# Kernel optimization log

Measured on AMD Instinct MI355X. Metric: run time of the kernel, lower is better.

Reference implementation:

```python
import jax, jax.numpy as jnp
import numpy as np

UNITS = 1024
LEVELS = 16
CHUNK = UNITS // LEVELS  # 64


def cumsoftmax(x, mode):
    # softmax then cumsum along last axis; 'r2l' reverses before/after
    if mode == 'l2r':
        return jnp.cumsum(jax.nn.softmax(x, axis=-1), axis=-1)
    else:  # 'r2l'
        xr = x[..., ::-1]
        return jnp.cumsum(jax.nn.softmax(xr, axis=-1), axis=-1)[..., ::-1]


def setup_inputs() -> dict:
    key = jax.random.key(0)
    k1, k2, k3 = jax.random.split(key, 3)
    B, T, D = 32, 512, 1024
    G = UNITS * 4 + LEVELS * 2  # 4128
    x = jax.random.normal(k1, (B, T, D), dtype=jnp.float32)
    kernel = jax.random.normal(k2, (D, G), dtype=jnp.float32) * (1.0 / np.sqrt(D))
    recurrent_kernel = jax.random.normal(k3, (UNITS, G), dtype=jnp.float32) * (1.0 / np.sqrt(UNITS))
    bias = jnp.zeros((G,), dtype=jnp.float32)
    return {"x": x, "kernel": kernel, "recurrent_kernel": recurrent_kernel, "bias": bias}


def reference(x, kernel, recurrent_kernel, bias):
    B, T, D = x.shape
    L, U, C = LEVELS, UNITS, CHUNK

    def one_step(carry, x_t):
        c_last, h_last = carry  # [B, U] each
        z = x_t @ kernel + h_last @ recurrent_kernel + bias  # [B, 4U+2L]
        f_master = cumsoftmax(z[:, :L], 'l2r')[:, :, None]       # [B, L, 1]
        i_master = cumsoftmax(z[:, L:2 * L], 'r2l')[:, :, None]  # [B, L, 1]
        g = z[:, 2 * L:].reshape(B, 4 * L, C)
        f_gate = jax.nn.sigmoid(g[:, :L])
        i_gate = jax.nn.sigmoid(g[:, L:2 * L])
        o_gate = jax.nn.sigmoid(g[:, 2 * L:3 * L])
        c_in = jnp.tanh(g[:, 3 * L:])
        c_prev = c_last.reshape(B, L, C)
        overlap = f_master * i_master
        c_out = (overlap * (f_gate * c_prev + i_gate * c_in)
                 + (f_master - overlap) * c_prev
                 + (i_master - overlap) * c_in)
        h_out = (o_gate * jnp.tanh(c_out)).reshape(B, U)
        c_out = c_out.reshape(B, U)
        return (c_out, h_out), h_out

    init = (jnp.zeros((B, U), x.dtype), jnp.zeros((B, U), x.dtype))
    _, h_seq = jax.lax.scan(one_step, init, jnp.swapaxes(x, 0, 1))  # [T, B, U]
    return jnp.swapaxes(h_seq, 0, 1)  # [B, T, U] (return_sequences=True)
```

## Files before the change

kernel.cpp:

```cpp
#include <hip/hip_runtime.h>

#define TT 512
#define GG 4128
#define GPAD 4224
#define NBLK2 64
#define NTHR2 512

typedef _Float16 f16;
typedef _Float16 half8 __attribute__((ext_vector_type(8)));
typedef _Float16 half4 __attribute__((ext_vector_type(4)));
typedef float f32x4 __attribute__((ext_vector_type(4)));
typedef unsigned long long ull;

__device__ __forceinline__ half8 h8(uint4 v) {
  union { uint4 u; half8 h; } c; c.u = v; return c.h;
}

__global__ void k_transpose_cvt(const float* __restrict__ in, f16* __restrict__ out,
                                int R, int C) {
  __shared__ float tile[32][33];
  int bx = blockIdx.x * 32, by = blockIdx.y * 32;
  int tx = threadIdx.x & 31, ty = threadIdx.x >> 5;
#pragma unroll
  for (int j = 0; j < 4; ++j) {
    int r = by + ty + j * 8;
    tile[ty + j * 8][tx] = in[(long)r * C + bx + tx];
  }
  __syncthreads();
#pragma unroll
  for (int j = 0; j < 4; ++j) {
    int c = bx + ty + j * 8;
    out[(long)c * R + by + tx] = (f16)tile[tx][ty + j * 8];
  }
}

__global__ __launch_bounds__(256) void k_gemm_xw(
    const float* __restrict__ X,
    const f16* __restrict__ Bt,
    const float* __restrict__ bias,
    f16* __restrict__ Zm,
    f16* __restrict__ Zg) {
  __shared__ f16 As[128 * 32];
  __shared__ f16 Bs[128 * 32];
  const int m0 = blockIdx.x * 128;
  const int n0 = blockIdx.y * 128;
  const int tid = threadIdx.x;
  const int wave = tid >> 6, lane = tid & 63;
  const int mrow = (wave & 1) * 64, ncol = (wave >> 1) * 64;
  f32x4 acc[4][4];
#pragma unroll
  for (int i = 0; i < 4; ++i)
#pragma unroll
    for (int j = 0; j < 4; ++j)
      acc[i][j] = (f32x4){0.f, 0.f, 0.f, 0.f};

  float4 ra[4];
  uint4 rb[2];
  auto load_tiles = [&](int k0) {
#pragma unroll
    for (int q = 0; q < 4; ++q) {
      int flat = q * 256 + tid;
      int r = flat >> 3, s = flat & 7;
      ra[q] = *(const float4*)(X + (long)(m0 + r) * 1024 + k0 + s * 4);
    }
#pragma unroll
    for (int q = 0; q < 2; ++q) {
      int flat = q * 256 + tid;
      int r = flat >> 2, s = flat & 3;
      rb[q] = *(const uint4*)(Bt + (long)(n0 + r) * 1024 + k0 + s * 8);
    }
  };
  load_tiles(0);
  for (int kt = 0; kt < 32; ++kt) {
    __syncthreads();
#pragma unroll
    for (int q = 0; q < 4; ++q) {
      int flat = q * 256 + tid;
      half4 h;
      h[0] = (f16)ra[q].x; h[1] = (f16)ra[q].y;
      h[2] = (f16)ra[q].z; h[3] = (f16)ra[q].w;
      *(half4*)((char*)As + flat * 8) = h;
    }
#pragma unroll
    for (int q = 0; q < 2; ++q) {
      int flat = q * 256 + tid;
      *(uint4*)((char*)Bs + flat * 16) = rb[q];
    }
    __syncthreads();
    if (kt + 1 < 32) load_tiles((kt + 1) * 32);
    const int kseg2 = ((lane >> 4) * 8) * 2;
    half8 af[4], bf[4];
#pragma unroll
    for (int i = 0; i < 4; ++i) {
      int r = mrow + i * 16 + (lane & 15);
      af[i] = *(const half8*)((const char*)As + r * 64 + kseg2);
      int c = ncol + i * 16 + (lane & 15);
      bf[i] = *(const half8*)((const char*)Bs + c * 64 + kseg2);
    }
#pragma unroll
    for (int i = 0; i < 4; ++i)
#pragma unroll
      for (int j = 0; j < 4; ++j)
        acc[i][j] = __builtin_amdgcn_mfma_f32_16x16x32_f16(af[i], bf[j], acc[i][j], 0, 0, 0);
  }
#pragma unroll
  for (int j = 0; j < 4; ++j) {
    int n = n0 + ncol + j * 16 + (lane & 15);
    if (n < GG) {
      float bv = bias[n];
      const int isM = (n < 32);
      int q = 0, u4 = 0, g2 = 0;
      if (!isM) {
        int k = n - 32;
        q = k >> 10;
        int u = k & 1023;
        g2 = u >> 4;
        u4 = u & 15;
      }
#pragma unroll
      for (int i = 0; i < 4; ++i) {
#pragma unroll
        for (int r = 0; r < 4; ++r) {
          int m = m0 + mrow + i * 16 + (lane >> 4) * 4 + r;
          int b = m >> 9, tt2 = m & 511;
          f16 v = (f16)(acc[i][j][r] + bv);
          if (isM)
            Zm[((long)(tt2 * 32 + b)) * 32 + n] = v;
          else
            Zg[((((long)tt2 * 64 + g2) * 32 + b) * 16 + u4) * 4 + q] = v;
        }
      }
    }
  }
}

__device__ __forceinline__ float sigm(float x) { return 1.f / (1.f + __expf(-x)); }
__device__ __forceinline__ float tanh_(float x) {
  float ax = fabsf(x);
  float e = __expf(-2.f * ax);
  float t = (1.f - e) / (1.f + e);
  return copysignf(t, x);
}
#define AG_LD(p) __hip_atomic_load((p), __ATOMIC_RELAXED, __HIP_MEMORY_SCOPE_AGENT)
#define AG_ST(p, v) __hip_atomic_store((p), (v), __ATOMIC_RELAXED, __HIP_MEMORY_SCOPE_AGENT)

__device__ __forceinline__ void bar_lds() {
  asm volatile("s_waitcnt lgkmcnt(0)" ::: "memory");
  __builtin_amdgcn_sched_barrier(0);
  __builtin_amdgcn_s_barrier();
  __builtin_amdgcn_sched_barrier(0);
}

__global__ __launch_bounds__(NTHR2, 2) void k_onlstm(
    const f16* __restrict__ Zm, const f16* __restrict__ Zg,
    const f16* __restrict__ Rt, unsigned* __restrict__ hbuf,
    unsigned* __restrict__ flags, float* __restrict__ Y) {
  extern __shared__ char lds[];
  float* cumlds = (float*)(lds + 32768);
  const int g = blockIdx.x, tid = threadIdx.x;
  const int wave = tid >> 6, lane = tid & 63;
  const int lr = lane & 15, lq = lane >> 4;
  const int kq = wave;
  const int b = tid >> 4;
  const int u = tid & 15;
  const int L0 = g >> 2;
  const int side = tid >> 5, mb = tid & 31;

  uint4 bq[16], bm[8];
  {
    const f16* base = Rt + (long)kq * 128 + lq * 8;
#pragma unroll
    for (int q = 0; q < 4; ++q)
#pragma unroll
      for (int ks = 0; ks < 4; ++ks)
        bq[q * 4 + ks] = *(const uint4*)(base + (long)(32 + q * 1024 + g * 16 + lr) * 1024 + ks * 32);
#pragma unroll
    for (int ct = 0; ct < 2; ++ct)
#pragma unroll
      for (int ks = 0; ks < 4; ++ks)
        bm[ct * 4 + ks] = *(const uint4*)(base + (long)(ct * 16 + lr) * 1024 + ks * 32);
#pragma unroll
    for (int i = 0; i < 16; ++i)
      asm volatile("" : "+v"(bq[i].x), "+v"(bq[i].y), "+v"(bq[i].z), "+v"(bq[i].w));
#pragma unroll
    for (int i = 0; i < 8; ++i)
      asm volatile("" : "+v"(bm[i].x), "+v"(bm[i].y), "+v"(bm[i].z), "+v"(bm[i].w));
  }
  float creg = 0.f;

  for (int t = 0; t < TT; ++t) {
    half4 zxh = *(const half4*)(Zg + ((((long)t * 64 + g) * 32 + b) * 16 + u) * 4);
    half8 zmr0, zmr1;
    if (wave == 0) {
      const half8* zmp = (const half8*)(Zm + ((long)t * 32 + mb) * 32 + side * 16);
      zmr0 = zmp[0];
      zmr1 = zmp[1];
    }
    if (t > 0) {
      for (;;) {
        unsigned v = AG_LD(flags + lane * 16);
        if (__all((int)(v >= (unsigned)t))) break;
      }
    }
    const ull* hrd = (const ull*)hbuf + (t & 1) * 8192;
    ull hv[16];
#pragma unroll
    for (int it = 0; it < 16; ++it)
      hv[it] = AG_LD(hrd + it * 512 + tid);
    __builtin_amdgcn_sched_barrier(0);
#pragma unroll
    for (int it = 0; it < 16; ++it) {
      int idx = it * 512 + tid;
      int bb = idx >> 8, j8 = idx & 255;
      *(ull*)(lds + ((bb * 128 + ((j8 >> 1) ^ (bb & 7))) << 4) + (j8 & 1) * 8) = hv[it];
    }
    bar_lds();
    f32x4 acc[4][2], accm[2][2];
#pragma unroll
    for (int q = 0; q < 4; ++q) {
      acc[q][0] = (f32x4){0.f, 0.f, 0.f, 0.f};
      acc[q][1] = (f32x4){0.f, 0.f, 0.f, 0.f};
    }
#pragma unroll
    for (int ct = 0; ct < 2; ++ct) {
      accm[ct][0] = (f32x4){0.f, 0.f, 0.f, 0.f};
      accm[ct][1] = (f32x4){0.f, 0.f, 0.f, 0.f};
    }
#pragma unroll
    for (int ks = 0; ks < 4; ++ks) {
      int ch = kq * 16 + ks * 4 + lq;
      half8 a0 = *(const half8*)(lds + ((lr * 128 + (ch ^ (lr & 7))) << 4));
      half8 a1 = *(const half8*)(lds + (((16 + lr) * 128 + (ch ^ ((16 + lr) & 7))) << 4));
#pragma unroll
      for (int q = 0; q < 4; ++q) {
        acc[q][0] = __builtin_amdgcn_mfma_f32_16x16x32_f16(a0, h8(bq[q * 4 + ks]), acc[q][0], 0, 0, 0);
        acc[q][1] = __builtin_amdgcn_mfma_f32_16x16x32_f16(a1, h8(bq[q * 4 + ks]), acc[q][1], 0, 0, 0);
      }
#pragma unroll
      for (int ct = 0; ct < 2; ++ct) {
        accm[ct][0] = __builtin_amdgcn_mfma_f32_16x16x32_f16(a0, h8(bm[ct * 4 + ks]), accm[ct][0], 0, 0, 0);
        accm[ct][1] = __builtin_amdgcn_mfma_f32_16x16x32_f16(a1, h8(bm[ct * 4 + ks]), accm[ct][1], 0, 0, 0);
      }
    }
#pragma unroll
    for (int q = 0; q < 4; ++q)
#pragma unroll
      for (int bt = 0; bt < 2; ++bt) {
        int bsw = (bt * 16 + lq * 4) ^ ((lr & 7) << 2);
        *(f32x4*)(lds + 65536 + (((kq * 64 + q * 16 + lr) * 32 + bsw) << 2)) = acc[q][bt];
      }
    bar_lds();
#pragma unroll
    for (int ct = 0; ct < 2; ++ct)
#pragma unroll
      for (int bt = 0; bt < 2; ++bt) {
        int col = ct * 16 + lr;
        int bsw = (bt * 16 + lq * 4) ^ ((col & 7) << 2);
        *(f32x4*)(lds + (((kq * 32 + col) * 32 + bsw) << 2)) = accm[ct][bt];
      }
    float z[4];
#pragma unroll
    for (int q = 0; q < 4; ++q) {
      float s = 0.f;
      int bsw = b ^ ((u & 7) << 2);
#pragma unroll
      for (int k8 = 0; k8 < 8; ++k8)
        s += *(const float*)(lds + 65536 + (((k8 * 64 + q * 16 + u) * 32 + bsw) << 2));
      z[q] = s + (float)zxh[q];
    }
    float f = sigm(z[0]), i_ = sigm(z[1]), o = sigm(z[2]);
    float ci = tanh_(z[3]);
    bar_lds();
    if (wave == 0) {
      float v[16];
#pragma unroll
      for (int j = 0; j < 16; ++j) {
        int col = side * 16 + j;
        int bsw = mb ^ ((col & 7) << 2);
        float s = 0.f;
#pragma unroll
        for (int k8 = 0; k8 < 8; ++k8)
          s += *(const float*)(lds + (((k8 * 32 + col) * 32 + bsw) << 2));
        v[j] = s + (float)((j < 8) ? zmr0[j] : zmr1[j - 8]);
      }
      float mx = v[0];
#pragma unroll
      for (int j = 1; j < 16; ++j) mx = fmaxf(mx, v[j]);
      float ssum = 0.f, p = 0.f;
#pragma unroll
      for (int j = 0; j < 16; ++j) {
        float e = __expf(v[j] - mx);
        ssum += e;
        bool take = side ? (j >= L0) : (j <= L0);
        if (take) p += e;
      }
      cumlds[side * 32 + mb] = p / ssum;
    }
    bar_lds();
    float fm = cumlds[b], im = cumlds[32 + b];
    float ov = fm * im;
    float cn = ov * (f * creg + i_ * ci) + (fm - ov) * creg + (im - ov) * ci;
    creg = cn;
    float hval = o * tanh_(cn);
    float hp = __shfl_xor(hval, 1);
    if (!(u & 1)) {
      union { f16 h[2]; unsigned w; } pk;
      pk.h[0] = (f16)hval;
      pk.h[1] = (f16)hp;
      AG_ST(hbuf + ((t + 1) & 1) * 16384 + b * 512 + g * 8 + (u >> 1), pk.w);
    }
    asm volatile("s_waitcnt vmcnt(0)" ::: "memory");
    __builtin_amdgcn_s_barrier();
    if (tid == 0) AG_ST(flags + g * 16, (unsigned)(t + 1));
    Y[((long)b * TT + t) * 1024 + g * 16 + u] = hval;
  }
}

extern "C" void kernel_launch(void* const* d_in, const int* in_sizes, int n_in,
                              void* d_out, int out_size, void* d_ws, size_t ws_size,
                              hipStream_t stream) {
  const float* X = (const float*)d_in[0];
  const float* W = (const float*)d_in[1];
  const float* Rm = (const float*)d_in[2];
  const float* bias = (const float*)d_in[3];
  float* Y = (float*)d_out;
  char* ws = (char*)d_ws;

  const size_t off_flags = 0;
  const size_t off_h = 4096;
  const size_t off_Zm = 135168;
  const size_t off_Wt = 1183744;
  const size_t off_Rt = 9834496;
  const size_t off_Zg = 18288640;
  const size_t need = off_Zg + (size_t)TT * 64 * 32 * 16 * 4 * 2;
  if (ws_size < need) return;

  unsigned* flags = (unsigned*)(ws + off_flags);
  unsigned* hbuf = (unsigned*)(ws + off_h);
  f16* Zm = (f16*)(ws + off_Zm);
  f16* Wt = (f16*)(ws + off_Wt);
  f16* Rt = (f16*)(ws + off_Rt);
  f16* Zg = (f16*)(ws + off_Zg);

  hipMemsetAsync(ws, 0, 135168, stream);
  hipMemsetAsync(ws + off_Wt + (size_t)GG * 1024 * 2, 0, (size_t)(GPAD - GG) * 1024 * 2, stream);

  k_transpose_cvt<<<dim3(129, 32), 256, 0, stream>>>(W, Wt, 1024, GG);
  k_transpose_cvt<<<dim3(129, 32), 256, 0, stream>>>(Rm, Rt, 1024, GG);
  k_gemm_xw<<<dim3(128, 33), 256, 0, stream>>>(X, Wt, bias, Zm, Zg);

  hipFuncSetAttribute((const void*)k_onlstm, hipFuncAttributeMaxDynamicSharedMemorySize, 131072);
  k_onlstm<<<NBLK2, NTHR2, 131072, stream>>>(Zm, Zg, Rt, hbuf, flags, Y);
}
```

Before: 4.204 ms.

## Embed step tags in hidden-state words to replace flag-based grid sync

Drops the per-block flag array and the barrier-then-flag publish. Each thread now writes its hidden value as an fp32 word whose low 8 mantissa bits carry the step tag. Readers spin on coherent dwordx4 loads of the whole hidden buffer until every tag matches. This removes a full block barrier, a store drain and a separate flag round trip from each recurrent step. In exchange it doubles the hidden-state traffic (fp32 instead of fp16), re-reads the whole buffer on every spin, and slightly truncates precision.

```diff
diff --git a/kernel.cpp b/kernel.cpp
--- a/kernel.cpp
+++ b/kernel.cpp
@@ -10,10 +10,18 @@
 typedef _Float16 half8 __attribute__((ext_vector_type(8)));
 typedef _Float16 half4 __attribute__((ext_vector_type(4)));
 typedef float f32x4 __attribute__((ext_vector_type(4)));
+typedef unsigned u32x4 __attribute__((ext_vector_type(4)));
 typedef unsigned long long ull;
 
 __device__ __forceinline__ half8 h8(uint4 v) {
   union { uint4 u; half8 h; } c; c.u = v; return c.h;
+}
+
+__device__ __forceinline__ u32x4 ld_cohx4(const unsigned* p) {
+  u32x4 r;
+  asm volatile("global_load_dwordx4 %0, %1, off sc0 sc1"
+               : "=v"(r) : "v"(p) : "memory");
+  return r;
 }
 
 __global__ void k_transpose_cvt(const float* __restrict__ in, f16* __restrict__ out,
@@ -141,7 +149,6 @@
   float t = (1.f - e) / (1.f + e);
   return copysignf(t, x);
 }
-#define AG_LD(p) __hip_atomic_load((p), __ATOMIC_RELAXED, __HIP_MEMORY_SCOPE_AGENT)
 #define AG_ST(p, v) __hip_atomic_store((p), (v), __ATOMIC_RELAXED, __HIP_MEMORY_SCOPE_AGENT)
 
 __device__ __forceinline__ void bar_lds() {
@@ -153,8 +160,8 @@
 
 __global__ __launch_bounds__(NTHR2, 2) void k_onlstm(
     const f16* __restrict__ Zm, const f16* __restrict__ Zg,
-    const f16* __restrict__ Rt, unsigned* __restrict__ hbuf,
-    unsigned* __restrict__ flags, float* __restrict__ Y) {
+    const f16* __restrict__ Rt, unsigned* __restrict__ hbuf32,
+    float* __restrict__ Y) {
   extern __shared__ char lds[];
   float* cumlds = (float*)(lds + 32768);
   const int g = blockIdx.x, tid = threadIdx.x;
@@ -196,23 +203,31 @@
       zmr0 = zmp[0];
       zmr1 = zmp[1];
     }
-    if (t > 0) {
-      for (;;) {
-        unsigned v = AG_LD(flags + lane * 16);
-        if (__all((int)(v >= (unsigned)t))) break;
-      }
-    }
-    const ull* hrd = (const ull*)hbuf + (t & 1) * 8192;
-    ull hv[16];
-#pragma unroll
-    for (int it = 0; it < 16; ++it)
-      hv[it] = AG_LD(hrd + it * 512 + tid);
-    __builtin_amdgcn_sched_barrier(0);
+    const unsigned* hb = hbuf32 + (t & 1) * 32768;
+    const unsigned tg = (unsigned)(t & 0xFF);
+    u32x4 hw[16];
+    for (;;) {
+#pragma unroll
+      for (int it = 0; it < 16; ++it)
+        hw[it] = ld_cohx4(hb + (it * 512 + tid) * 4);
+      asm volatile("s_waitcnt vmcnt(0)" ::: "memory");
+      __builtin_amdgcn_sched_barrier(0);
+      unsigned bad = 0;
+#pragma unroll
+      for (int it = 0; it < 16; ++it)
+        bad |= (hw[it].x ^ tg) | (hw[it].y ^ tg) | (hw[it].z ^ tg) | (hw[it].w ^ tg);
+      if (__all((int)((bad & 0xFFu) == 0u))) break;
+    }
 #pragma unroll
     for (int it = 0; it < 16; ++it) {
       int idx = it * 512 + tid;
       int bb = idx >> 8, j8 = idx & 255;
-      *(ull*)(lds + ((bb * 128 + ((j8 >> 1) ^ (bb & 7))) << 4) + (j8 & 1) * 8) = hv[it];
+      half4 hh;
+      hh[0] = (f16)__uint_as_float(hw[it].x);
+      hh[1] = (f16)__uint_as_float(hw[it].y);
+      hh[2] = (f16)__uint_as_float(hw[it].z);
+      hh[3] = (f16)__uint_as_float(hw[it].w);
+      *(half4*)(lds + ((bb * 128 + ((j8 >> 1) ^ (bb & 7))) << 4) + (j8 & 1) * 8) = hh;
     }
     bar_lds();
     f32x4 acc[4][2], accm[2][2];
@@ -302,16 +317,8 @@
     float cn = ov * (f * creg + i_ * ci) + (fm - ov) * creg + (im - ov) * ci;
     creg = cn;
     float hval = o * tanh_(cn);
-    float hp = __shfl_xor(hval, 1);
-    if (!(u & 1)) {
-      union { f16 h[2]; unsigned w; } pk;
-      pk.h[0] = (f16)hval;
-      pk.h[1] = (f16)hp;
-      AG_ST(hbuf + ((t + 1) & 1) * 16384 + b * 512 + g * 8 + (u >> 1), pk.w);
-    }
-    asm volatile("s_waitcnt vmcnt(0)" ::: "memory");
-    __builtin_amdgcn_s_barrier();
-    if (tid == 0) AG_ST(flags + g * 16, (unsigned)(t + 1));
+    unsigned hword = (__float_as_uint(hval) & 0xFFFFFF00u) | ((unsigned)(t + 1) & 0xFFu);
+    AG_ST(hbuf32 + ((t + 1) & 1) * 32768 + b * 1024 + g * 16 + u, hword);
     Y[((long)b * TT + t) * 1024 + g * 16 + u] = hval;
   }
 }
@@ -326,23 +333,21 @@
   float* Y = (float*)d_out;
   char* ws = (char*)d_ws;
 
-  const size_t off_flags = 0;
-  const size_t off_h = 4096;
-  const size_t off_Zm = 135168;
-  const size_t off_Wt = 1183744;
-  const size_t off_Rt = 9834496;
-  const size_t off_Zg = 18288640;
+  const size_t off_h = 0;
+  const size_t off_Zm = 262144;
+  const size_t off_Wt = 1310720;
+  const size_t off_Rt = 9961472;
+  const size_t off_Zg = 18415616;
   const size_t need = off_Zg + (size_t)TT * 64 * 32 * 16 * 4 * 2;
   if (ws_size < need) return;
 
-  unsigned* flags = (unsigned*)(ws + off_flags);
-  unsigned* hbuf = (unsigned*)(ws + off_h);
+  unsigned* hbuf32 = (unsigned*)(ws + off_h);
   f16* Zm = (f16*)(ws + off_Zm);
   f16* Wt = (f16*)(ws + off_Wt);
   f16* Rt = (f16*)(ws + off_Rt);
   f16* Zg = (f16*)(ws + off_Zg);
 
-  hipMemsetAsync(ws, 0, 135168, stream);
+  hipMemsetAsync(ws + off_h, 0, 262144, stream);
   hipMemsetAsync(ws + off_Wt + (size_t)GG * 1024 * 2, 0, (size_t)(GPAD - GG) * 1024 * 2, stream);
 
   k_transpose_cvt<<<dim3(129, 32), 256, 0, stream>>>(W, Wt, 1024, GG);
@@ -350,5 +355,5 @@
   k_gemm_xw<<<dim3(128, 33), 256, 0, stream>>>(X, Wt, bias, Zm, Zg);
 
   hipFuncSetAttribute((const void*)k_onlstm, hipFuncAttributeMaxDynamicSharedMemorySize, 131072);
-  k_onlstm<<<NBLK2, NTHR2, 131072, stream>>>(Zm, Zg, Rt, hbuf, flags, Y);
-}
+  k_onlstm<<<NBLK2, NTHR2, 131072, stream>>>(Zm, Zg, Rt, hbuf32, Y);
+}
```

After: 3.833 ms. 1.1x faster.

## Load recurrent h straight into MFMA registers and compute master gates in every thread

Applied to the files above, without the earlier changes.

Each wave now reads its MFMA A-operand fragments of h directly from global memory using coherent dwordx4 loads, so the LDS staging of h and its barrier are gone. The master-gate reductions are now spread across all threads and written to LDS. Every thread then recomputes the two 16-wide cumsoftmax values for its batch row instead of having wave 0 compute them and broadcast them. This removes one block barrier per timestep and the serial wave-0 softmax section on the recurrent critical path, at the cost of redundant exp work and more global load traffic per wave.

```diff
diff --git a/kernel.cpp b/kernel.cpp
--- a/kernel.cpp
+++ b/kernel.cpp
@@ -10,10 +10,21 @@
 typedef _Float16 half8 __attribute__((ext_vector_type(8)));
 typedef _Float16 half4 __attribute__((ext_vector_type(4)));
 typedef float f32x4 __attribute__((ext_vector_type(4)));
+typedef unsigned u32x4 __attribute__((ext_vector_type(4)));
 typedef unsigned long long ull;
 
 __device__ __forceinline__ half8 h8(uint4 v) {
   union { uint4 u; half8 h; } c; c.u = v; return c.h;
+}
+__device__ __forceinline__ half8 h8v(u32x4 v) {
+  union { u32x4 u; half8 h; } c; c.u = v; return c.h;
+}
+
+__device__ __forceinline__ u32x4 ld_cohx4(const unsigned* p) {
+  u32x4 r;
+  asm volatile("global_load_dwordx4 %0, %1, off sc0 sc1"
+               : "=v"(r) : "v"(p) : "memory");
+  return r;
 }
 
 __global__ void k_transpose_cvt(const float* __restrict__ in, f16* __restrict__ out,
@@ -154,9 +165,8 @@
 __global__ __launch_bounds__(NTHR2, 2) void k_onlstm(
     const f16* __restrict__ Zm, const f16* __restrict__ Zg,
     const f16* __restrict__ Rt, unsigned* __restrict__ hbuf,
-    unsigned* __restrict__ flags, float* __restrict__ Y) {
+    unsigned* __restrict__ flagbuf, float* __restrict__ Y) {
   extern __shared__ char lds[];
-  float* cumlds = (float*)(lds + 32768);
   const int g = blockIdx.x, tid = threadIdx.x;
   const int wave = tid >> 6, lane = tid & 63;
   const int lr = lane & 15, lq = lane >> 4;
@@ -164,21 +174,21 @@
   const int b = tid >> 4;
   const int u = tid & 15;
   const int L0 = g >> 2;
-  const int side = tid >> 5, mb = tid & 31;
+  const int rb_ = tid & 31, rc = tid >> 5;
 
   uint4 bq[16], bm[8];
   {
-    const f16* base = Rt + (long)kq * 128 + lq * 8;
+    const f16* baseg = Rt + (long)kq * 128 + lq * 8;
 #pragma unroll
     for (int q = 0; q < 4; ++q)
 #pragma unroll
       for (int ks = 0; ks < 4; ++ks)
-        bq[q * 4 + ks] = *(const uint4*)(base + (long)(32 + q * 1024 + g * 16 + lr) * 1024 + ks * 32);
+        bq[q * 4 + ks] = *(const uint4*)(baseg + (long)(32 + q * 1024 + g * 16 + lr) * 1024 + ks * 32);
 #pragma unroll
     for (int ct = 0; ct < 2; ++ct)
 #pragma unroll
       for (int ks = 0; ks < 4; ++ks)
-        bm[ct * 4 + ks] = *(const uint4*)(base + (long)(ct * 16 + lr) * 1024 + ks * 32);
+        bm[ct * 4 + ks] = *(const uint4*)(baseg + (long)(ct * 16 + lr) * 1024 + ks * 32);
 #pragma unroll
     for (int i = 0; i < 16; ++i)
       asm volatile("" : "+v"(bq[i].x), "+v"(bq[i].y), "+v"(bq[i].z), "+v"(bq[i].w));
@@ -187,34 +197,29 @@
       asm volatile("" : "+v"(bm[i].x), "+v"(bm[i].y), "+v"(bm[i].z), "+v"(bm[i].w));
   }
   float creg = 0.f;
+  const int wb0 = lr * 512 + kq * 64 + lq * 4;
+  const int wb1 = (lr + 16) * 512 + kq * 64 + lq * 4;
 
   for (int t = 0; t < TT; ++t) {
     half4 zxh = *(const half4*)(Zg + ((((long)t * 64 + g) * 32 + b) * 16 + u) * 4);
-    half8 zmr0, zmr1;
-    if (wave == 0) {
-      const half8* zmp = (const half8*)(Zm + ((long)t * 32 + mb) * 32 + side * 16);
-      zmr0 = zmp[0];
-      zmr1 = zmp[1];
-    }
+    f16 zm0 = Zm[((long)t * 32 + rb_) * 32 + rc];
+    f16 zm1 = Zm[((long)t * 32 + rb_) * 32 + rc + 16];
     if (t > 0) {
+      const unsigned tg = (unsigned)t;
       for (;;) {
-        unsigned v = AG_LD(flags + lane * 16);
-        if (__all((int)(v >= (unsigned)t))) break;
-      }
-    }
-    const ull* hrd = (const ull*)hbuf + (t & 1) * 8192;
-    ull hv[16];
-#pragma unroll
-    for (int it = 0; it < 16; ++it)
-      hv[it] = AG_LD(hrd + it * 512 + tid);
+        unsigned v = AG_LD(flagbuf + lane * 16);
+        if (__all((int)(v >= tg))) break;
+      }
+    }
+    const unsigned* hb = hbuf + (t & 1) * 16384;
+    u32x4 ha[8];
+#pragma unroll
+    for (int ks = 0; ks < 4; ++ks) {
+      ha[ks] = ld_cohx4(hb + wb0 + ks * 16);
+      ha[4 + ks] = ld_cohx4(hb + wb1 + ks * 16);
+    }
+    asm volatile("s_waitcnt vmcnt(0)" ::: "memory");
     __builtin_amdgcn_sched_barrier(0);
-#pragma unroll
-    for (int it = 0; it < 16; ++it) {
-      int idx = it * 512 + tid;
-      int bb = idx >> 8, j8 = idx & 255;
-      *(ull*)(lds + ((bb * 128 + ((j8 >> 1) ^ (bb & 7))) << 4) + (j8 & 1) * 8) = hv[it];
-    }
-    bar_lds();
     f32x4 acc[4][2], accm[2][2];
 #pragma unroll
     for (int q = 0; q < 4; ++q) {
@@ -228,9 +233,8 @@
     }
 #pragma unroll
     for (int ks = 0; ks < 4; ++ks) {
-      int ch = kq * 16 + ks * 4 + lq;
-      half8 a0 = *(const half8*)(lds + ((lr * 128 + (ch ^ (lr & 7))) << 4));
-      half8 a1 = *(const half8*)(lds + (((16 + lr) * 128 + (ch ^ ((16 + lr) & 7))) << 4));
+      half8 a0 = h8v(ha[ks]);
+      half8 a1 = h8v(ha[4 + ks]);
 #pragma unroll
       for (int q = 0; q < 4; ++q) {
         acc[q][0] = __builtin_amdgcn_mfma_f32_16x16x32_f16(a0, h8(bq[q * 4 + ks]), acc[q][0], 0, 0, 0);
@@ -247,57 +251,64 @@
 #pragma unroll
       for (int bt = 0; bt < 2; ++bt) {
         int bsw = (bt * 16 + lq * 4) ^ ((lr & 7) << 2);
-        *(f32x4*)(lds + 65536 + (((kq * 64 + q * 16 + lr) * 32 + bsw) << 2)) = acc[q][bt];
+        *(f32x4*)(lds + (((kq * 64 + q * 16 + lr) * 32 + bsw) << 2)) = acc[q][bt];
+      }
+#pragma unroll
+    for (int ct = 0; ct < 2; ++ct)
+#pragma unroll
+      for (int bt = 0; bt < 2; ++bt) {
+        int colm = ct * 16 + lr;
+        int bsw = (bt * 16 + lq * 4) ^ ((colm & 7) << 2);
+        *(f32x4*)(lds + 65536 + (((kq * 32 + colm) * 32 + bsw) << 2)) = accm[ct][bt];
       }
     bar_lds();
-#pragma unroll
-    for (int ct = 0; ct < 2; ++ct)
-#pragma unroll
-      for (int bt = 0; bt < 2; ++bt) {
-        int col = ct * 16 + lr;
-        int bsw = (bt * 16 + lq * 4) ^ ((col & 7) << 2);
-        *(f32x4*)(lds + (((kq * 32 + col) * 32 + bsw) << 2)) = accm[ct][bt];
-      }
     float z[4];
-#pragma unroll
-    for (int q = 0; q < 4; ++q) {
+    {
+      int bswg = b ^ ((u & 7) << 2);
+#pragma unroll
+      for (int q = 0; q < 4; ++q) {
+        float s = 0.f;
+#pragma unroll
+        for (int k8 = 0; k8 < 8; ++k8)
+          s += *(const float*)(lds + (((k8 * 64 + q * 16 + u) * 32 + bswg) << 2));
+        z[q] = s + (float)zxh[q];
+      }
+    }
+#pragma unroll
+    for (int rep = 0; rep < 2; ++rep) {
+      int c = rc + rep * 16;
+      int bswm = rb_ ^ ((c & 7) << 2);
       float s = 0.f;
-      int bsw = b ^ ((u & 7) << 2);
 #pragma unroll
       for (int k8 = 0; k8 < 8; ++k8)
-        s += *(const float*)(lds + 65536 + (((k8 * 64 + q * 16 + u) * 32 + bsw) << 2));
-      z[q] = s + (float)zxh[q];
-    }
+        s += *(const float*)(lds + 65536 + (((k8 * 32 + c) * 32 + bswm) << 2));
+      s += (float)(rep ? zm1 : zm0);
+      *(float*)(lds + 98304 + ((c * 32 + bswm) << 2)) = s;
+    }
+    bar_lds();
+    float vf[16], vi[16];
+#pragma unroll
+    for (int j = 0; j < 16; ++j) {
+      int bsw = b ^ ((j & 7) << 2);
+      vf[j] = *(const float*)(lds + 98304 + (((j * 32) + bsw) << 2));
+      vi[j] = *(const float*)(lds + 98304 + ((((16 + j) * 32) + bsw) << 2));
+    }
+    float mf = vf[0], mi = vi[0];
+#pragma unroll
+    for (int j = 1; j < 16; ++j) { mf = fmaxf(mf, vf[j]); mi = fmaxf(mi, vi[j]); }
+    float sf = 0.f, pf = 0.f, si = 0.f, pi = 0.f;
+#pragma unroll
+    for (int j = 0; j < 16; ++j) {
+      float ef = __expf(vf[j] - mf);
+      sf += ef;
+      if (j <= L0) pf += ef;
+      float ei = __expf(vi[j] - mi);
+      si += ei;
+      if (j >= L0) pi += ei;
+    }
+    float fm = pf / sf, im = pi / si;
     float f = sigm(z[0]), i_ = sigm(z[1]), o = sigm(z[2]);
     float ci = tanh_(z[3]);
-    bar_lds();
-    if (wave == 0) {
-      float v[16];
-#pragma unroll
-      for (int j = 0; j < 16; ++j) {
-        int col = side * 16 + j;
-        int bsw = mb ^ ((col & 7) << 2);
-        float s = 0.f;
-#pragma unroll
-        for (int k8 = 0; k8 < 8; ++k8)
-          s += *(const float*)(lds + (((k8 * 32 + col) * 32 + bsw) << 2));
-        v[j] = s + (float)((j < 8) ? zmr0[j] : zmr1[j - 8]);
-      }
-      float mx = v[0];
-#pragma unroll
-      for (int j = 1; j < 16; ++j) mx = fmaxf(mx, v[j]);
-      float ssum = 0.f, p = 0.f;
-#pragma unroll
-      for (int j = 0; j < 16; ++j) {
-        float e = __expf(v[j] - mx);
-        ssum += e;
-        bool take = side ? (j >= L0) : (j <= L0);
-        if (take) p += e;
-      }
-      cumlds[side * 32 + mb] = p / ssum;
-    }
-    bar_lds();
-    float fm = cumlds[b], im = cumlds[32 + b];
     float ov = fm * im;
     float cn = ov * (f * creg + i_ * ci) + (fm - ov) * creg + (im - ov) * ci;
     creg = cn;
@@ -311,7 +322,7 @@
     }
     asm volatile("s_waitcnt vmcnt(0)" ::: "memory");
     __builtin_amdgcn_s_barrier();
-    if (tid == 0) AG_ST(flags + g * 16, (unsigned)(t + 1));
+    if (tid == 0) AG_ST(flagbuf + g * 16, (unsigned)(t + 1));
     Y[((long)b * TT + t) * 1024 + g * 16 + u] = hval;
   }
 }
@@ -335,7 +346,7 @@
   const size_t need = off_Zg + (size_t)TT * 64 * 32 * 16 * 4 * 2;
   if (ws_size < need) return;
 
-  unsigned* flags = (unsigned*)(ws + off_flags);
+  unsigned* flagbuf = (unsigned*)(ws + off_flags);
   unsigned* hbuf = (unsigned*)(ws + off_h);
   f16* Zm = (f16*)(ws + off_Zm);
   f16* Wt = (f16*)(ws + off_Wt);
@@ -349,6 +360,6 @@
   k_transpose_cvt<<<dim3(129, 32), 256, 0, stream>>>(Rm, Rt, 1024, GG);
   k_gemm_xw<<<dim3(128, 33), 256, 0, stream>>>(X, Wt, bias, Zm, Zg);
 
-  hipFuncSetAttribute((const void*)k_onlstm, hipFuncAttributeMaxDynamicSharedMemorySize, 131072);
-  k_onlstm<<<NBLK2, NTHR2, 131072, stream>>>(Zm, Zg, Rt, hbuf, flags, Y);
-}
+  hipFuncSetAttribute((const void*)k_onlstm, hipFuncAttributeMaxDynamicSharedMemorySize, 102400);
+  k_onlstm<<<NBLK2, NTHR2, 102400, stream>>>(Zm, Zg, Rt, hbuf, flagbuf, Y);
+}
```

After: 3.750 ms (median of 2 runs). 1.12x faster.
